# Optimization experiments

Measured on AMD Instinct MI355X. Metric: run time of the kernel, lower is better.

The kernel has to match this reference:

```python
import jax, jax.numpy as jnp
import numpy as np

N, E, H = 100000, 3200000, 128


def setup_inputs() -> dict:
    key = jax.random.key(0)
    ks = jax.random.split(key, 12)
    s = 1.0 / np.sqrt(H)
    x = jax.random.normal(ks[0], (N, H), dtype=jnp.float32)
    edge_index = jax.random.randint(ks[1], (2, E), 0, N, dtype=jnp.int64)
    # GatedGraphConv weight: [num_layers=1, H, H] -> single [H, H]
    W = jax.random.normal(ks[2], (H, H), dtype=jnp.float32) * s
    # GRUCell (gate order: r, z, n)
    gru_w_ih = jax.random.normal(ks[3], (3 * H, H), dtype=jnp.float32) * s
    gru_w_hh = jax.random.normal(ks[4], (3 * H, H), dtype=jnp.float32) * s
    gru_b_ih = jax.random.normal(ks[5], (3 * H,), dtype=jnp.float32) * s
    gru_b_hh = jax.random.normal(ks[6], (3 * H,), dtype=jnp.float32) * s
    # LSTM layer 0 (gate order: i, f, g, o)
    lstm_w_ih = jax.random.normal(ks[7], (4 * H, H), dtype=jnp.float32) * s
    lstm_w_hh = jax.random.normal(ks[8], (4 * H, H), dtype=jnp.float32) * s
    lstm_b_ih = jax.random.normal(ks[9], (4 * H,), dtype=jnp.float32) * s
    lstm_b_hh = jax.random.normal(ks[10], (4 * H,), dtype=jnp.float32) * s
    return {
        "x": x, "edge_index": edge_index, "W": W,
        "gru_w_ih": gru_w_ih, "gru_w_hh": gru_w_hh,
        "gru_b_ih": gru_b_ih, "gru_b_hh": gru_b_hh,
        "lstm_w_ih": lstm_w_ih, "lstm_w_hh": lstm_w_hh,
        "lstm_b_ih": lstm_b_ih, "lstm_b_hh": lstm_b_hh,
    }


def _forward(x, edge_index, W, gru_w_ih, gru_w_hh, gru_b_ih, gru_b_hh,
             lstm_w_ih, lstm_w_hh, lstm_b_ih, lstm_b_hh):
    n = x.shape[0]
    src, dst = edge_index[0], edge_index[1]
    # GatedGraphConv, num_layers=1, mean aggregation
    m = x @ W                                   # [N, H]
    msg = m[src]                                # [E, H] gather (memory-bound)
    agg_sum = jax.ops.segment_sum(msg, dst, num_segments=n)
    deg = jax.ops.segment_sum(jnp.ones((src.shape[0],), x.dtype), dst, num_segments=n)
    agg = agg_sum / jnp.maximum(deg, 1.0)[:, None]
    # GRUCell(agg, x): gates r, z, n
    gi = agg @ gru_w_ih.T + gru_b_ih
    gh = x @ gru_w_hh.T + gru_b_hh
    i_r, i_z, i_n = jnp.split(gi, 3, axis=-1)
    h_r, h_z, h_n = jnp.split(gh, 3, axis=-1)
    r = jax.nn.sigmoid(i_r + h_r)
    z = jax.nn.sigmoid(i_z + h_z)
    ng = jnp.tanh(i_n + r * h_n)
    h_conv = (1.0 - z) * ng + z * x             # conv output H_tilde
    # 1-layer LSTM over seq_len=1 with zero initial (H, C)
    gates = h_conv @ lstm_w_ih.T + lstm_b_ih + lstm_b_hh  # h0 = 0
    i_g, f_g, g_g, o_g = jnp.split(gates, 4, axis=-1)
    c = jax.nn.sigmoid(i_g) * jnp.tanh(g_g)
    h_lstm = jax.nn.sigmoid(o_g) * jnp.tanh(c)
    return jax.nn.relu(h_lstm)


def reference(x, edge_index, W, gru_w_ih, gru_w_hh, gru_b_ih, gru_b_hh,
              lstm_w_ih, lstm_w_hh, lstm_b_ih, lstm_b_hh):
    return _forward(x, edge_index, W, gru_w_ih, gru_w_hh, gru_b_ih, gru_b_hh,
                    lstm_w_ih, lstm_w_hh, lstm_b_ih, lstm_b_hh)
```

## Files before the change

### kernel.cpp

```cpp
#include <hip/hip_runtime.h>
#include <math.h>

#define HD 128
#define PB 256
#define SCB 4096

typedef __attribute__((ext_vector_type(8))) short short8;
typedef __attribute__((ext_vector_type(4))) float f32x4;
typedef __attribute__((ext_vector_type(2))) float f32x2;
typedef __attribute__((ext_vector_type(4))) unsigned u32x4;

__device__ __forceinline__ float sigf(float v) { return 1.0f / (1.0f + __expf(-v)); }
__device__ __forceinline__ float tanhf_fast(float v) {
  float e = __expf(2.0f * v);
  return 1.0f - 2.0f / (e + 1.0f);
}

__device__ __forceinline__ unsigned short f2bf(float f) {
  union { float f; unsigned u; } v; v.f = f;
  unsigned r = (v.u + 0x7fffu + ((v.u >> 16) & 1u)) >> 16;
  return (unsigned short)r;
}
__device__ __forceinline__ float bf2f(unsigned short b) {
  union { unsigned u; float f; } v; v.u = ((unsigned)b) << 16;
  return v.f;
}


__global__ __launch_bounds__(256) void bcount_k(const int* __restrict__ ei,
                                                int* __restrict__ bcnt,
                                                int E, int N, int shift, int NB) {
  __shared__ int h[256];
  const int blk = blockIdx.x, tid = threadIdx.x;
  h[tid] = 0;
  __syncthreads();
  int per = (E + PB - 1) / PB;
  int lo = blk * per;
  int hi = (lo + per < E) ? lo + per : E;
  for (int e = lo + tid; e < hi; e += 256) {
    int d = ei[(size_t)E + e];
    if ((unsigned)d >= (unsigned)N) continue;
    atomicAdd(&h[d >> shift], 1);
  }
  __syncthreads();
  if (tid < NB) bcnt[tid * PB + blk] = h[tid];
}

__global__ __launch_bounds__(256) void scan1_k(const int* __restrict__ a,
                                               int* __restrict__ bsums, int total) {
  __shared__ int ts[256];
  int b = blockIdx.x, tid = threadIdx.x;
  int lo = b * SCB + tid * 16;
  int s = 0;
#pragma unroll
  for (int i = 0; i < 16; ++i) {
    int idx = lo + i;
    if (idx < total) s += a[idx];
  }
  ts[tid] = s;
  __syncthreads();
  for (int off = 128; off > 0; off >>= 1) {
    if (tid < off) ts[tid] += ts[tid + off];
    __syncthreads();
  }
  if (tid == 0) bsums[b] = ts[0];
}

__global__ __launch_bounds__(256) void scan2_k(int* __restrict__ bsums, int nb) {
  __shared__ int ts[256];
  int tid = threadIdx.x;
  int v = (tid < nb) ? bsums[tid] : 0;
  ts[tid] = v;
  __syncthreads();
  for (int off = 1; off < 256; off <<= 1) {
    int u = (tid >= off) ? ts[tid - off] : 0;
    __syncthreads();
    ts[tid] += u;
    __syncthreads();
  }
  if (tid < nb) bsums[tid] = ts[tid] - v;
}

__global__ __launch_bounds__(256) void scan3_k(int* __restrict__ a,
                                               const int* __restrict__ bsums,
                                               int total, int nblk) {
  __shared__ int ts[256];
  int b = blockIdx.x, tid = threadIdx.x;
  int lo = b * SCB + tid * 16;
  int pre[16];
  int s = 0;
#pragma unroll
  for (int i = 0; i < 16; ++i) {
    int idx = lo + i;
    int xv = (idx < total) ? a[idx] : 0;
    pre[i] = s;
    s += xv;
  }
  ts[tid] = s;
  __syncthreads();
  for (int off = 1; off < 256; off <<= 1) {
    int u = (tid >= off) ? ts[tid - off] : 0;
    __syncthreads();
    ts[tid] += u;
    __syncthreads();
  }
  int off0 = ts[tid] - s + bsums[b];
#pragma unroll
  for (int i = 0; i < 16; ++i) {
    int idx = lo + i;
    if (idx < total) a[idx] = off0 + pre[i];
  }
  if (b == nblk - 1 && tid == 255) a[total] = off0 + s;
}

__global__ __launch_bounds__(256) void bpart_k(const int* __restrict__ ei,
                                               const int* __restrict__ bstart,
                                               unsigned* __restrict__ ebuf,
                                               int E, int N, int shift, int NB,
                                               int sbits) {
  __shared__ int cur[256];
  const int blk = blockIdx.x, tid = threadIdx.x;
  if (tid < NB) cur[tid] = bstart[tid * PB + blk];
  __syncthreads();
  int per = (E + PB - 1) / PB;
  int lo = blk * per;
  int hi = (lo + per < E) ? lo + per : E;
  const unsigned dmask = (1u << shift) - 1u;
  for (int e = lo + tid; e < hi; e += 256) {
    int s = ei[e];
    int d = ei[(size_t)E + e];
    if ((unsigned)s >= (unsigned)N || (unsigned)d >= (unsigned)N) continue;
    int p = atomicAdd(&cur[d >> shift], 1);
    ebuf[p] = (((unsigned)d & dmask) << sbits) | (unsigned)s;
  }
}

__global__ __launch_bounds__(256) void bfill2_k(const unsigned* __restrict__ ebuf,
                                                const int* __restrict__ bstart,
                                                int* __restrict__ rowstart,
                                                int* __restrict__ csr,
                                                int N, int shift, int NB, int sbits) {
  __shared__ int cnt[2048];
  __shared__ int tsum[256];
  const int b = blockIdx.x, tid = threadIdx.x;
  const int d0 = b << shift;
  int dmax = d0 + (1 << shift);
  if (dmax > N) dmax = N;
  const int nd = dmax - d0;
  const unsigned smask = (1u << sbits) - 1u;
  for (int i = tid; i < nd; i += 256) cnt[i] = 0;
  __syncthreads();
  const int base = bstart[b * PB];
  const int end = bstart[(b + 1) * PB];
  for (int idx = base + tid; idx < end; idx += 256)
    atomicAdd(&cnt[ebuf[idx] >> sbits], 1);
  __syncthreads();
  const int C = (nd + 255) / 256;
  int lo = tid * C;
  int hi = (lo + C < nd) ? lo + C : nd;
  int loc[8];
  int s = 0;
  for (int i = lo; i < hi; ++i) {
    loc[i - lo] = cnt[i];
    s += cnt[i];
  }
  tsum[tid] = s;
  __syncthreads();
  for (int off = 1; off < 256; off <<= 1) {
    int u = (tid >= off) ? tsum[tid - off] : 0;
    __syncthreads();
    tsum[tid] += u;
    __syncthreads();
  }
  int run = tsum[tid] - s + base;
  for (int i = lo; i < hi; ++i) {
    rowstart[d0 + i] = run;
    cnt[i] = run;
    run += loc[i - lo];
  }
  if (b == NB - 1 && tid == 255) rowstart[N] = end;
  __syncthreads();
  for (int idx = base + tid; idx < end; idx += 256) {
    unsigned pk = ebuf[idx];
    int p = atomicAdd(&cnt[pk >> sbits], 1);
    csr[p] = (int)(pk & smask);
  }
}

__global__ __launch_bounds__(256) void prep_k(
    const float* __restrict__ x, unsigned short* __restrict__ xb,
    unsigned* __restrict__ x8,
    const float* __restrict__ gwhh, const float* __restrict__ lwih,
    const float* __restrict__ lbih, const float* __restrict__ lbhh,
    unsigned short* __restrict__ gwhhb, unsigned short* __restrict__ lwb,
    float* __restrict__ lbias,
    const float* __restrict__ W, const float* __restrict__ gwih,
    unsigned short* __restrict__ Bpb, int n4) {
  int t = blockIdx.x * 256 + threadIdx.x;
  if (t < n4) {
    float4 v = reinterpret_cast<const float4*>(x)[t];
    ushort4 o;
    o.x = f2bf(v.x); o.y = f2bf(v.y); o.z = f2bf(v.z); o.w = f2bf(v.w);
    reinterpret_cast<ushort4*>(xb)[t] = o;
    int p8 = 0;
    p8 = __builtin_amdgcn_cvt_pk_fp8_f32(v.x, v.y, p8, false);
    p8 = __builtin_amdgcn_cvt_pk_fp8_f32(v.z, v.w, p8, true);
    x8[t] = (unsigned)p8;
    return;
  }
  t -= n4;
  if (t < 49152) { gwhhb[t] = f2bf(gwhh[t]); return; }
  t -= 49152;
  if (t < 49152) {
    int j = t >> 7, k = t & 127;
    int jm = j < 128 ? j : j + 128;
    lwb[t] = f2bf(lwih[(size_t)jm * 128 + k]);
    return;
  }
  t -= 49152;
  if (t < 384) {
    int jm = t < 128 ? t : t + 128;
    lbias[t] = lbih[jm] + lbhh[jm];
    return;
  }
  t -= 384;
  if (t < 49152) {
    int j = t >> 7, k = t & 127;
    const float4* wr = reinterpret_cast<const float4*>(W + (size_t)k * 128);
    const float4* gr = reinterpret_cast<const float4*>(gwih + (size_t)j * 128);
    float acc = 0.f;
#pragma unroll
    for (int c = 0; c < 32; ++c) {
      float4 a = wr[c], b = gr[c];
      acc += a.x * b.x + a.y * b.y + a.z * b.z + a.w * b.w;
    }
    Bpb[t] = f2bf(acc);
  }
}

__device__ __forceinline__ void accf8(f32x2* acc, uint4 v) {
  acc[0] += __builtin_amdgcn_cvt_pk_f32_fp8((int)v.x, false);
  acc[1] += __builtin_amdgcn_cvt_pk_f32_fp8((int)v.x, true);
  acc[2] += __builtin_amdgcn_cvt_pk_f32_fp8((int)v.y, false);
  acc[3] += __builtin_amdgcn_cvt_pk_f32_fp8((int)v.y, true);
  acc[4] += __builtin_amdgcn_cvt_pk_f32_fp8((int)v.z, false);
  acc[5] += __builtin_amdgcn_cvt_pk_f32_fp8((int)v.z, true);
  acc[6] += __builtin_amdgcn_cvt_pk_f32_fp8((int)v.w, false);
  acc[7] += __builtin_amdgcn_cvt_pk_f32_fp8((int)v.w, true);
}

__global__ __launch_bounds__(256) void gather_f8_k(const int* __restrict__ csr,
                                                   const int* __restrict__ rowstart,
                                                   const unsigned* __restrict__ x8,
                                                   unsigned short* __restrict__ xaggb, int N) {
  int w = (int)(((long long)blockIdx.x * 256 + threadIdx.x) >> 6);
  if (w >= N) return;
  const int lane = threadIdx.x & 63;
  const int sub = lane >> 3, li = lane & 7;
  const int beg = rowstart[w], end = rowstart[w + 1];
  const uint4* x4 = reinterpret_cast<const uint4*>(x8);

  f32x2 acc[8];
#pragma unroll
  for (int i = 0; i < 8; ++i) acc[i] = (f32x2)0.f;

  const int nfull = (end - beg) >> 4;
  uint4 v0, v1;
  if (nfull > 0) {
    int s0 = __builtin_nontemporal_load(&csr[beg + sub]);
    int s1 = __builtin_nontemporal_load(&csr[beg + 8 + sub]);
    v0 = x4[(size_t)s0 * 8 + li];
    v1 = x4[(size_t)s1 * 8 + li];
  }
  for (int it = 1; it < nfull; ++it) {
    int jn = beg + it * 16;
    int s0 = __builtin_nontemporal_load(&csr[jn + sub]);
    int s1 = __builtin_nontemporal_load(&csr[jn + 8 + sub]);
    uint4 n0 = x4[(size_t)s0 * 8 + li];
    uint4 n1 = x4[(size_t)s1 * 8 + li];
    accf8(acc, v0);
    accf8(acc, v1);
    v0 = n0;
    v1 = n1;
  }
  if (nfull > 0) {
    accf8(acc, v0);
    accf8(acc, v1);
  }
  int j = beg + nfull * 16;
  if (j + 8 <= end) {
    int s0 = __builtin_nontemporal_load(&csr[j + sub]);
    uint4 t0 = x4[(size_t)s0 * 8 + li];
    accf8(acc, t0);
    j += 8;
  }
  int rem = end - j;
  if (sub < rem) {
    int s0 = csr[j + sub];
    uint4 t0 = x4[(size_t)s0 * 8 + li];
    accf8(acc, t0);
  }

  float a16[16];
#pragma unroll
  for (int i = 0; i < 8; ++i) { a16[2 * i] = acc[i].x; a16[2 * i + 1] = acc[i].y; }
#pragma unroll
  for (int i = 0; i < 16; ++i) {
    a16[i] += __shfl_xor(a16[i], 8, 64);
    a16[i] += __shfl_xor(a16[i], 16, 64);
    a16[i] += __shfl_xor(a16[i], 32, 64);
  }

  if (lane < 8) {
    float scale = 1.0f / fmaxf((float)(end - beg), 1.0f);
    u32x4 o1, o2;
    o1.x = (unsigned)f2bf(a16[0] * scale) | ((unsigned)f2bf(a16[1] * scale) << 16);
    o1.y = (unsigned)f2bf(a16[2] * scale) | ((unsigned)f2bf(a16[3] * scale) << 16);
    o1.z = (unsigned)f2bf(a16[4] * scale) | ((unsigned)f2bf(a16[5] * scale) << 16);
    o1.w = (unsigned)f2bf(a16[6] * scale) | ((unsigned)f2bf(a16[7] * scale) << 16);
    o2.x = (unsigned)f2bf(a16[8] * scale) | ((unsigned)f2bf(a16[9] * scale) << 16);
    o2.y = (unsigned)f2bf(a16[10] * scale) | ((unsigned)f2bf(a16[11] * scale) << 16);
    o2.z = (unsigned)f2bf(a16[12] * scale) | ((unsigned)f2bf(a16[13] * scale) << 16);
    o2.w = (unsigned)f2bf(a16[14] * scale) | ((unsigned)f2bf(a16[15] * scale) << 16);
    u32x4* dst = reinterpret_cast<u32x4*>(xaggb + (size_t)w * HD) + li * 2;
    __builtin_nontemporal_store(o1, dst);
    __builtin_nontemporal_store(o2, dst + 1);
  }
}

__global__ __launch_bounds__(256) void gru_fused_k(
    const unsigned short* __restrict__ xaggb, const unsigned short* __restrict__ xb,
    const unsigned short* __restrict__ Bpb, const unsigned short* __restrict__ gwhhb,
    const float* __restrict__ gbih, const float* __restrict__ gbhh,
    unsigned short* __restrict__ hconv, int nrows) {
  __shared__ unsigned short Bsm[6][32][136];
  const int tid = threadIdx.x;
  const int w = tid >> 6, lane = tid & 63;
  const int q = lane >> 4, r = lane & 15;
  const int row0 = blockIdx.y * 64;
  const int c0 = blockIdx.x * 32;

#pragma unroll
  for (int it = 0; it < 12; ++it) {
    int idx = it * 256 + tid;
    int p = idx >> 9;
    int rem = idx & 511;
    int col = rem >> 4, kq = rem & 15;
    const unsigned short* src =
        (p < 3) ? Bpb + ((size_t)(p * 128 + c0 + col)) * HD
                : gwhhb + ((size_t)((p - 3) * 128 + c0 + col)) * HD;
    uint4 v = *reinterpret_cast<const uint4*>(src + kq * 8);
    *reinterpret_cast<uint4*>(&Bsm[p][col][kq * 8]) = v;
  }
  __syncthreads();

  int arow = row0 + (w << 4) + r;
  int ar = arow < nrows ? arow : nrows - 1;
  const unsigned short* Aa = xaggb + (size_t)ar * HD + q * 8;
  const unsigned short* Ax = xb + (size_t)ar * HD + q * 8;

  f32x4 acc[6][2];
#pragma unroll
  for (int p = 0; p < 6; ++p)
#pragma unroll
    for (int cb = 0; cb < 2; ++cb) acc[p][cb] = (f32x4)0.f;

#pragma unroll
  for (int ks = 0; ks < 4; ++ks) {
    short8 a1 = *reinterpret_cast<const short8*>(Aa + ks * 32);
    short8 a2 = *reinterpret_cast<const short8*>(Ax + ks * 32);
#pragma unroll
    for (int p = 0; p < 6; ++p) {
      short8 af = (p < 3) ? a1 : a2;
#pragma unroll
      for (int cb = 0; cb < 2; ++cb) {
        short8 bf = *reinterpret_cast<const short8*>(&Bsm[p][cb * 16 + r][ks * 32 + q * 8]);
        acc[p][cb] = __builtin_amdgcn_mfma_f32_16x16x32_bf16(af, bf, acc[p][cb], 0, 0, 0);
      }
    }
  }

#pragma unroll
  for (int cb = 0; cb < 2; ++cb) {
    int col = c0 + cb * 16 + r;
    float bir = gbih[col], biz = gbih[col + 128], bin = gbih[col + 256];
    float bhr = gbhh[col], bhz = gbhh[col + 128], bhn = gbhh[col + 256];
#pragma unroll
    for (int reg = 0; reg < 4; ++reg) {
      int row = row0 + (w << 4) + q * 4 + reg;
      if (row < nrows) {
        float ir = acc[0][cb][reg] + bir, iz = acc[1][cb][reg] + biz;
        float inn = acc[2][cb][reg] + bin;
        float hr = acc[3][cb][reg] + bhr, hz = acc[4][cb][reg] + bhz;
        float hn = acc[5][cb][reg] + bhn;
        float rr = sigf(ir + hr), zz = sigf(iz + hz);
        float nn = tanhf_fast(inn + rr * hn);
        float xv = bf2f(xb[(size_t)row * HD + col]);
        hconv[(size_t)row * HD + col] = f2bf((1.f - zz) * nn + zz * xv);
      }
    }
  }
}

__global__ __launch_bounds__(256) void lstm_fused_k(
    const unsigned short* __restrict__ hconv, const unsigned short* __restrict__ lwb,
    const float* __restrict__ lbias, float* __restrict__ out, int nrows) {
  __shared__ unsigned short Bsm[3][64][136];
  const int tid = threadIdx.x;
  const int w = tid >> 6, lane = tid & 63;
  const int q = lane >> 4, r = lane & 15;
  const int row0 = blockIdx.y * 64;
  const int c0 = blockIdx.x * 64;

#pragma unroll
  for (int it = 0; it < 12; ++it) {
    int idx = it * 256 + tid;
    int p = idx >> 10, rem = idx & 1023;
    int col = rem >> 4, kq = rem & 15;
    uint4 v = *reinterpret_cast<const uint4*>(
        lwb + ((size_t)(p * 128 + c0 + col)) * HD + kq * 8);
    *reinterpret_cast<uint4*>(&Bsm[p][col][kq * 8]) = v;
  }
  __syncthreads();

  int arow = row0 + (w << 4) + r;
  int ar = arow < nrows ? arow : nrows - 1;
  const unsigned short* Ap = hconv + (size_t)ar * HD + q * 8;

  f32x4 acc[3][4];
#pragma unroll
  for (int p = 0; p < 3; ++p)
#pragma unroll
    for (int cb = 0; cb < 4; ++cb) acc[p][cb] = (f32x4)0.f;

#pragma unroll
  for (int ks = 0; ks < 4; ++ks) {
    short8 af = *reinterpret_cast<const short8*>(Ap + ks * 32);
#pragma unroll
    for (int p = 0; p < 3; ++p)
#pragma unroll
      for (int cb = 0; cb < 4; ++cb) {
        short8 bf = *reinterpret_cast<const short8*>(&Bsm[p][cb * 16 + r][ks * 32 + q * 8]);
        acc[p][cb] = __builtin_amdgcn_mfma_f32_16x16x32_bf16(af, bf, acc[p][cb], 0, 0, 0);
      }
  }

#pragma unroll
  for (int cb = 0; cb < 4; ++cb) {
    int col = c0 + cb * 16 + r;
    float bi = lbias[col], bg = lbias[col + 128], bo = lbias[col + 256];
#pragma unroll
    for (int reg = 0; reg < 4; ++reg) {
      int row = row0 + (w << 4) + q * 4 + reg;
      if (row < nrows) {
        float ig = acc[0][cb][reg] + bi;
        float gg = acc[1][cb][reg] + bg;
        float og = acc[2][cb][reg] + bo;
        float cc = sigf(ig) * tanhf_fast(gg);
        out[(size_t)row * HD + col] = fmaxf(sigf(og) * tanhf_fast(cc), 0.f);
      }
    }
  }
}


extern "C" void kernel_launch(void* const* d_in, const int* in_sizes, int n_in,
                              void* d_out, int out_size, void* d_ws, size_t ws_size,
                              hipStream_t stream) {
  const float* x = (const float*)d_in[0];
  const int* ei = (const int*)d_in[1];
  const float* W = (const float*)d_in[2];
  const float* gw_ih = (const float*)d_in[3];
  const float* gw_hh = (const float*)d_in[4];
  const float* gb_ih = (const float*)d_in[5];
  const float* gb_hh = (const float*)d_in[6];
  const float* lw_ih = (const float*)d_in[7];
  const float* lb_ih = (const float*)d_in[9];
  const float* lb_hh = (const float*)d_in[10];
  float* out = (float*)d_out;

  const int N = in_sizes[0] / HD;
  const int E = in_sizes[1] / 2;
  const size_t nH = (size_t)N * HD;

  int shift = 9;
  while (((N + (1 << shift) - 1) >> shift) > 256) ++shift;
  const int NB = (N + (1 << shift) - 1) >> shift;
  const int sbits = 32 - shift;

  const size_t N4p = (size_t)((N + 1 + 7) & ~7);
  const size_t E4 = (size_t)((E + 3) & ~3);
  const size_t BC = (size_t)NB * PB + 8;
  const int sc_total = NB * PB;
  const int sc_nblk = (sc_total + SCB - 1) / SCB;

  char* p = (char*)d_ws;
  int* rowstart = (int*)p;  p += 4 * N4p;
  int* bcnt = (int*)p;      p += 4 * BC;
  int* bsums = (int*)p;     p += 4 * 64;
  int* csr = (int*)p;       p += 4 * E4;
  size_t sz_eb = 4 * E4, sz_xb = 2 * nH;
  unsigned* ebuf = (unsigned*)p;
  unsigned short* xb = (unsigned short*)p;
  p += (sz_eb > sz_xb ? sz_eb : sz_xb);
  unsigned short* hconv = (unsigned short*)p;  p += 2 * nH;
  unsigned short* Bpb = (unsigned short*)p;    p += 2 * 49152;
  unsigned short* gwhhb = (unsigned short*)p;  p += 2 * 49152;
  unsigned short* lwb = (unsigned short*)p;    p += 2 * 49152;
  float* lbias = (float*)p;                    p += 4 * 384;

  unsigned* x8 = (unsigned*)hconv;

  unsigned short* xaggb = (unsigned short*)d_out;

  dim3 blk(256);
  unsigned rb = (unsigned)((N + 63) / 64);

  bcount_k<<<PB, blk, 0, stream>>>(ei, bcnt, E, N, shift, NB);
  scan1_k<<<sc_nblk, blk, 0, stream>>>(bcnt, bsums, sc_total);
  scan2_k<<<1, blk, 0, stream>>>(bsums, sc_nblk);
  scan3_k<<<sc_nblk, blk, 0, stream>>>(bcnt, bsums, sc_total, sc_nblk);
  bpart_k<<<PB, blk, 0, stream>>>(ei, bcnt, ebuf, E, N, shift, NB, sbits);
  bfill2_k<<<NB, blk, 0, stream>>>(ebuf, bcnt, rowstart, csr, N, shift, NB, sbits);

  int n4 = (int)(nH / 4);
  int prep_total = n4 + 49152 + 49152 + 384 + 49152;
  prep_k<<<(unsigned)((prep_total + 255) / 256), blk, 0, stream>>>(
      x, xb, x8, gw_hh, lw_ih, lb_ih, lb_hh, gwhhb, lwb, lbias, W, gw_ih, Bpb, n4);

  long long gthreads = (long long)N * 64;
  gather_f8_k<<<(unsigned)((gthreads + 255) / 256), blk, 0, stream>>>(
      csr, rowstart, x8, xaggb, N);

  gru_fused_k<<<dim3(4, rb), blk, 0, stream>>>(
      xaggb, xb, Bpb, gwhhb, gb_ih, gb_hh, hconv, N);

  lstm_fused_k<<<dim3(2, rb), blk, 0, stream>>>(hconv, lwb, lbias, out, N);
}
```

Baseline: 470.8 us.

## Split gather into two half launches, simplify loop, double partition blocks

Splits the fp8 neighbor gather over two launches, each covering half the rows on the same stream. The software-pipelined prefetch loop becomes a plain loop over 16-edge and 8-edge chunks. The block count for the bucket count and partition kernels doubles from 256 to 512. Together these change gather scheduling and partition parallelism, at the cost of an extra launch, the loss of explicit load prefetching, and more per-block bucket-count state to scan.

New measurement: 468.8 us. Within noise of the previous version (-0.4%).

```diff
diff --git a/kernel.cpp b/kernel.cpp
--- a/kernel.cpp
+++ b/kernel.cpp
@@ -2,7 +2,7 @@
 #include <math.h>
 
 #define HD 128
-#define PB 256
+#define PB 512
 #define SCB 4096
 
 typedef __attribute__((ext_vector_type(8))) short short8;
@@ -252,9 +252,10 @@
 __global__ __launch_bounds__(256) void gather_f8_k(const int* __restrict__ csr,
                                                    const int* __restrict__ rowstart,
                                                    const unsigned* __restrict__ x8,
-                                                   unsigned short* __restrict__ xaggb, int N) {
-  int w = (int)(((long long)blockIdx.x * 256 + threadIdx.x) >> 6);
-  if (w >= N) return;
+                                                   unsigned short* __restrict__ xaggb,
+                                                   int row0, int rowend) {
+  int w = row0 + (int)(((long long)blockIdx.x * 256 + threadIdx.x) >> 6);
+  if (w >= rowend) return;
   const int lane = threadIdx.x & 63;
   const int sub = lane >> 3, li = lane & 7;
   const int beg = rowstart[w], end = rowstart[w + 1];
@@ -264,41 +265,25 @@
 #pragma unroll
   for (int i = 0; i < 8; ++i) acc[i] = (f32x2)0.f;
 
-  const int nfull = (end - beg) >> 4;
-  uint4 v0, v1;
-  if (nfull > 0) {
-    int s0 = __builtin_nontemporal_load(&csr[beg + sub]);
-    int s1 = __builtin_nontemporal_load(&csr[beg + 8 + sub]);
-    v0 = x4[(size_t)s0 * 8 + li];
-    v1 = x4[(size_t)s1 * 8 + li];
-  }
-  for (int it = 1; it < nfull; ++it) {
-    int jn = beg + it * 16;
-    int s0 = __builtin_nontemporal_load(&csr[jn + sub]);
-    int s1 = __builtin_nontemporal_load(&csr[jn + 8 + sub]);
-    uint4 n0 = x4[(size_t)s0 * 8 + li];
-    uint4 n1 = x4[(size_t)s1 * 8 + li];
+  int j = beg;
+  for (; j + 16 <= end; j += 16) {
+    int s0 = __builtin_nontemporal_load(&csr[j + sub]);
+    int s1 = __builtin_nontemporal_load(&csr[j + 8 + sub]);
+    uint4 v0 = x4[(size_t)s0 * 8 + li];
+    uint4 v1 = x4[(size_t)s1 * 8 + li];
     accf8(acc, v0);
     accf8(acc, v1);
-    v0 = n0;
-    v1 = n1;
-  }
-  if (nfull > 0) {
+  }
+  for (; j + 8 <= end; j += 8) {
+    int s0 = __builtin_nontemporal_load(&csr[j + sub]);
+    uint4 v0 = x4[(size_t)s0 * 8 + li];
     accf8(acc, v0);
-    accf8(acc, v1);
-  }
-  int j = beg + nfull * 16;
-  if (j + 8 <= end) {
-    int s0 = __builtin_nontemporal_load(&csr[j + sub]);
-    uint4 t0 = x4[(size_t)s0 * 8 + li];
-    accf8(acc, t0);
-    j += 8;
   }
   int rem = end - j;
   if (sub < rem) {
     int s0 = csr[j + sub];
-    uint4 t0 = x4[(size_t)s0 * 8 + li];
-    accf8(acc, t0);
+    uint4 v0 = x4[(size_t)s0 * 8 + li];
+    accf8(acc, v0);
   }
 
   float a16[16];
@@ -528,9 +513,15 @@
   prep_k<<<(unsigned)((prep_total + 255) / 256), blk, 0, stream>>>(
       x, xb, x8, gw_hh, lw_ih, lb_ih, lb_hh, gwhhb, lwb, lbias, W, gw_ih, Bpb, n4);
 
-  long long gthreads = (long long)N * 64;
-  gather_f8_k<<<(unsigned)((gthreads + 255) / 256), blk, 0, stream>>>(
-      csr, rowstart, x8, xaggb, N);
+  int half = N / 2;
+  {
+    long long gt0 = (long long)half * 64;
+    gather_f8_k<<<(unsigned)((gt0 + 255) / 256), blk, 0, stream>>>(
+        csr, rowstart, x8, xaggb, 0, half);
+    long long gt1 = (long long)(N - half) * 64;
+    gather_f8_k<<<(unsigned)((gt1 + 255) / 256), blk, 0, stream>>>(
+        csr, rowstart, x8, xaggb, half, N);
+  }
 
   gru_fused_k<<<dim3(4, rb), blk, 0, stream>>>(
       xaggb, xb, Bpb, gwhhb, gb_ih, gb_hh, hconv, N);
```
